# Kernel optimization log

Hardware: AMD Instinct MI355X
Metric: run time of the kernel (lower is better)

## Reference

```python
import jax, jax.numpy as jnp
import numpy as np

B, S, D, H = 2, 2048, 1024, 16
DK = D // H  # 64
ROPE_THETA = 10000.0


def apply_rope(t, positions):
    # t: [B, H, S, DK]; positions: [B, S]
    half = DK // 2
    inv_freq = 1.0 / (ROPE_THETA ** (jnp.arange(0, DK, 2, dtype=jnp.float32) / DK))  # [half]
    ang = positions.astype(jnp.float32)[:, None, :, None] * inv_freq  # [B,1,S,half]
    cos, sin = jnp.cos(ang), jnp.sin(ang)
    t_even = t[..., 0::2]
    t_odd = t[..., 1::2]
    r_even = t_even * cos - t_odd * sin
    r_odd = t_even * sin + t_odd * cos
    # interleave back to original layout
    return jnp.stack([r_even, r_odd], axis=-1).reshape(t.shape)


def setup_inputs() -> dict:
    key = jax.random.key(0)
    ks = jax.random.split(key, 5)
    x = jax.random.normal(ks[0], (B, S, D), dtype=jnp.float32)
    token_positions = jnp.broadcast_to(jnp.arange(S, dtype=jnp.int64 if jax.config.jax_enable_x64 else jnp.int32), (B, S))
    w_q = jax.random.normal(ks[1], (D, D), dtype=jnp.float32)
    w_k = jax.random.normal(ks[2], (D, D), dtype=jnp.float32)
    w_v = jax.random.normal(ks[3], (D, D), dtype=jnp.float32)
    w_o = jax.random.normal(ks[4], (D, D), dtype=jnp.float32)
    return {"x": x, "token_positions": token_positions, "w_q": w_q, "w_k": w_k, "w_v": w_v, "w_o": w_o}


def reference(x, token_positions, w_q, w_k, w_v, w_o):
    # project: weights stored as (h*d_k, d_model)
    wq = w_q.reshape(H, DK, D)
    wk = w_k.reshape(H, DK, D)
    wv = w_v.reshape(H, DK, D)
    q = jnp.einsum('bsd,hkd->bhsk', x, wq)  # [B,H,S,DK]
    k = jnp.einsum('bsd,hkd->bhsk', x, wk)
    v = jnp.einsum('bsd,hkd->bhsk', x, wv)
    q = apply_rope(q, token_positions)
    k = apply_rope(k, token_positions)
    scale = 1.0 / jnp.sqrt(jnp.float32(DK))
    scores = jnp.einsum('bhnk,bhmk->bhnm', q, k) * scale  # [B,H,S,S]
    causal = jnp.tril(jnp.ones((S, S), dtype=bool))
    scores = jnp.where(causal, scores, -jnp.inf)
    attn = jax.nn.softmax(scores, axis=-1)
    out = jnp.einsum('bhnm,bhmv->bhnv', attn, v)  # [B,H,S,DK]
    out = jnp.transpose(out, (0, 2, 1, 3)).reshape(B, S, H * DK)
    return jnp.einsum('bsf,df->bsd', out, w_o)
```

## Files before the change

### kernel.cpp

```cpp
#include <hip/hip_runtime.h>

typedef unsigned short u16;
typedef unsigned int u32;
typedef __attribute__((ext_vector_type(8))) __bf16 bf16x8;
typedef __attribute__((ext_vector_type(4))) float f32x4;

#define NSEQ 2048
#define NDIM 1024
#define NHEAD 16
#define NTOK 4096
#define NX   4194304
#define NWEL 1048576

__device__ __forceinline__ u16 f2bf(float f) {
  unsigned u = __float_as_uint(f);
  return (u16)((u + 0x7fffu + ((u >> 16) & 1u)) >> 16);
}
__device__ __forceinline__ float bf2f(u16 h) {
  return __uint_as_float(((unsigned)h) << 16);
}
__device__ __forceinline__ bf16x8 ld16(const u16* p) {
  int4 v = *reinterpret_cast<const int4*>(p);
  return __builtin_bit_cast(bf16x8, v);
}
__device__ __forceinline__ f32x4 mfma16(bf16x8 a, bf16x8 b, f32x4 c) {
  return __builtin_amdgcn_mfma_f32_16x16x32_bf16(a, b, c, 0, 0, 0);
}
__device__ __forceinline__ u32 cvtpk(float lo, float hi) {
  u32 r;
  asm("v_cvt_pk_bf16_f32 %0, %1, %2" : "=v"(r) : "v"(lo), "v"(hi));
  return r;
}
__device__ __forceinline__ void gload16(const u16* g, u16* l) {
  __builtin_amdgcn_global_load_lds(
      (const __attribute__((address_space(1))) void*)g,
      (__attribute__((address_space(3))) void*)l, 16, 0, 0);
}

#define GEMM_PROLOGUE                                                         \
  const int tid = threadIdx.x;                                                \
  const int lane = tid & 63, wid = tid >> 6;                                  \
  const int wm = wid >> 1, wn = wid & 1;                                      \
  const int lr = lane & 15, lg = lane >> 4;                                   \
  const int srow_ = tid >> 2;                                                 \
  const int sch_ = ((tid & 3) ^ ((tid >> 3) & 3)) * 8;                        \
  const int rsw_ = (lg ^ ((lr >> 1) & 3)) * 8;

#define STAGE3(BB, AH, AL, BH, BL, T0, J0, K0)                                \
  {                                                                           \
    u16* bb_ = (BB);                                                          \
    gload16(AH + (size_t)((T0) + srow_) * NDIM + (K0) + sch_, bb_ + tid * 8); \
    gload16(AH + (size_t)((T0) + 64 + srow_) * NDIM + (K0) + sch_,            \
            bb_ + 2048 + tid * 8);                                            \
    gload16(BH + (size_t)((J0) + srow_) * NDIM + (K0) + sch_,                 \
            bb_ + 4096 + tid * 8);                                            \
    gload16(BH + (size_t)((J0) + 64 + srow_) * NDIM + (K0) + sch_,            \
            bb_ + 6144 + tid * 8);                                            \
    gload16(AL + (size_t)((T0) + srow_) * NDIM + (K0) + sch_,                 \
            bb_ + 8192 + tid * 8);                                            \
    gload16(AL + (size_t)((T0) + 64 + srow_) * NDIM + (K0) + sch_,            \
            bb_ + 10240 + tid * 8);                                           \
    gload16(BL + (size_t)((J0) + srow_) * NDIM + (K0) + sch_,                 \
            bb_ + 12288 + tid * 8);                                           \
    gload16(BL + (size_t)((J0) + 64 + srow_) * NDIM + (K0) + sch_,            \
            bb_ + 14336 + tid * 8);                                           \
  }

#define GEMM3_LOOP(AH, AL, BH, BL, T0, J0)                                    \
  STAGE3(lds, AH, AL, BH, BL, T0, J0, 0)                                      \
  __syncthreads();                                                            \
  for (int k0 = 0; k0 < NDIM; k0 += 32) {                                     \
    u16* cb_ = lds + ((k0 >> 5) & 1) * 16384;                                 \
    if (k0 + 32 < NDIM) {                                                     \
      u16* nb_ = lds + ((((k0 >> 5) & 1) ^ 1) * 16384);                       \
      STAGE3(nb_, AH, AL, BH, BL, T0, J0, k0 + 32)                            \
    }                                                                         \
    bf16x8 afh[4], afl[4];                                                    \
    _Pragma("unroll") for (int m = 0; m < 4; m++) {                           \
      int off = (wm * 64 + m * 16 + lr) * 32 + rsw_;                          \
      afh[m] = ld16(cb_ + off);                                               \
      afl[m] = ld16(cb_ + 8192 + off);                                        \
    }                                                                         \
    _Pragma("unroll") for (int n = 0; n < 4; n++) {                           \
      int off = (wn * 64 + n * 16 + lr) * 32 + rsw_;                          \
      bf16x8 bfh = ld16(cb_ + 4096 + off);                                    \
      bf16x8 bfl = ld16(cb_ + 12288 + off);                                   \
      _Pragma("unroll") for (int m = 0; m < 4; m++) {                         \
        acc[m][n] = mfma16(afh[m], bfh, acc[m][n]);                           \
        acc[m][n] = mfma16(afh[m], bfl, acc[m][n]);                           \
        acc[m][n] = mfma16(afl[m], bfh, acc[m][n]);                           \
      }                                                                       \
    }                                                                         \
    __syncthreads();                                                          \
  }

#define STAGE1(BB, AH, BH, T0, J0, K0)                                        \
  {                                                                           \
    u16* bb_ = (BB);                                                          \
    gload16(AH + (size_t)((T0) + srow_) * NDIM + (K0) + sch_, bb_ + tid * 8); \
    gload16(AH + (size_t)((T0) + 64 + srow_) * NDIM + (K0) + sch_,            \
            bb_ + 2048 + tid * 8);                                            \
    gload16(BH + (size_t)((J0) + srow_) * NDIM + (K0) + sch_,                 \
            bb_ + 4096 + tid * 8);                                            \
    gload16(BH + (size_t)((J0) + 64 + srow_) * NDIM + (K0) + sch_,            \
            bb_ + 6144 + tid * 8);                                            \
  }

#define GEMM1_LOOP(AH, BH, T0, J0)                                            \
  STAGE1(lds, AH, BH, T0, J0, 0)                                              \
  __syncthreads();                                                            \
  for (int k0 = 0; k0 < NDIM; k0 += 32) {                                     \
    u16* cb_ = lds + ((k0 >> 5) & 1) * 8192;                                  \
    if (k0 + 32 < NDIM) {                                                     \
      u16* nb_ = lds + ((((k0 >> 5) & 1) ^ 1) * 8192);                        \
      STAGE1(nb_, AH, BH, T0, J0, k0 + 32)                                    \
    }                                                                         \
    bf16x8 afh[4];                                                            \
    _Pragma("unroll") for (int m = 0; m < 4; m++) {                           \
      int off = (wm * 64 + m * 16 + lr) * 32 + rsw_;                          \
      afh[m] = ld16(cb_ + off);                                               \
    }                                                                         \
    _Pragma("unroll") for (int n = 0; n < 4; n++) {                           \
      int off = (wn * 64 + n * 16 + lr) * 32 + rsw_;                          \
      bf16x8 bfh = ld16(cb_ + 4096 + off);                                    \
      _Pragma("unroll") for (int m = 0; m < 4; m++) {                         \
        acc[m][n] = mfma16(afh[m], bfh, acc[m][n]);                           \
      }                                                                       \
    }                                                                         \
    __syncthreads();                                                          \
  }

__global__ __launch_bounds__(256) void k_prep(
    const float* __restrict__ x, const float* __restrict__ wq,
    const float* __restrict__ wk, const float* __restrict__ wv,
    const float* __restrict__ wo,
    u16* __restrict__ xh, u16* __restrict__ xl,
    u16* __restrict__ wh, u16* __restrict__ wl) {
  int g = blockIdx.x * 256 + threadIdx.x;
  const float4* src;
  u16 *dh, *dl;
  int idx;
  bool wantlo = true;
  if (g < NX / 4) {
    src = (const float4*)x; dh = xh; dl = xl; idx = g;
  } else {
    int z = (g - NX / 4) / (NWEL / 4);
    int r = (g - NX / 4) % (NWEL / 4);
    src = (const float4*)(z == 0 ? wq : z == 1 ? wk : z == 2 ? wv : wo);
    dh = wh + (size_t)z * NWEL; dl = wl + (size_t)z * NWEL; idx = r;
    wantlo = (z < 2);
  }
  float4 v = src[idx];
  u16 h0 = f2bf(v.x), h1 = f2bf(v.y), h2 = f2bf(v.z), h3 = f2bf(v.w);
  ushort4 hv = make_ushort4(h0, h1, h2, h3);
  ((ushort4*)dh)[idx] = hv;
  if (wantlo) {
    ushort4 lv = make_ushort4(f2bf(v.x - bf2f(h0)), f2bf(v.y - bf2f(h1)),
                              f2bf(v.z - bf2f(h2)), f2bf(v.w - bf2f(h3)));
    ((ushort4*)dl)[idx] = lv;
  }
}

__global__ __launch_bounds__(256) void k_tab(float2* __restrict__ csn) {
  int idx = blockIdx.x * 256 + threadIdx.x;
  int p = idx >> 5, j = idx & 31;
  double invf = exp((double)(2 * j) * (-9.210340371976184 / 64.0));
  double ang = (double)p * invf;
  double kq = rint(ang * 0.15915494309189535);
  float a = (float)(ang - kq * 6.283185307179586);
  csn[idx] = make_float2(cosf(a), sinf(a));
}

__global__ __launch_bounds__(256) void k_qkv(
    const u16* __restrict__ xh, const u16* __restrict__ xl,
    const u16* __restrict__ wh, const u16* __restrict__ wl,
    const int* __restrict__ tokpos, const float2* __restrict__ csn,
    u16* __restrict__ qh, u16* __restrict__ ql,
    u16* __restrict__ kh, u16* __restrict__ kl) {
  __shared__ __align__(16) u16 lds[32768];
  const int z = blockIdx.z;
  const int t0 = blockIdx.y * 128, j0 = blockIdx.x * 128;
  const int h0 = j0 >> 6;
  GEMM_PROLOGUE
  const u16* Bh = wh + (size_t)z * NWEL;
  const u16* Bl = wl + (size_t)z * NWEL;
  f32x4 acc[4][4];
#pragma unroll
  for (int m = 0; m < 4; m++)
#pragma unroll
    for (int n = 0; n < 4; n++) acc[m][n] = f32x4{0.f, 0.f, 0.f, 0.f};
  GEMM3_LOOP(xh, xl, Bh, Bl, t0, j0)

  const int b = t0 >> 11, s0 = t0 & 2047;
  u16* dh = (z == 0) ? qh : kh;
  u16* dl = (z == 0) ? ql : kl;
  float rv[4][4][4];
#pragma unroll
  for (int m = 0; m < 4; m++) {
#pragma unroll
    for (int r = 0; r < 4; r++) {
      int pos = tokpos[t0 + wm * 64 + m * 16 + lg * 4 + r];
#pragma unroll
      for (int n = 0; n < 4; n++) {
        float val = acc[m][n][r];
        float nb = __shfl_xor(val, 1);
        int dk = (wn * 64 + n * 16 + lr) & 63;
        float2 cs = csn[pos * 32 + (dk >> 1)];
        rv[m][r][n] = (dk & 1) ? (nb * cs.y + val * cs.x)
                               : (val * cs.x - nb * cs.y);
      }
    }
  }
#pragma unroll
  for (int pass = 0; pass < 2; pass++) {
    __syncthreads();
#pragma unroll
    for (int m = 0; m < 4; m++)
#pragma unroll
      for (int r = 0; r < 4; r++) {
        int rloc = wm * 64 + m * 16 + lg * 4 + r;
#pragma unroll
        for (int n = 0; n < 4; n++) {
          int cloc = wn * 64 + n * 16 + lr;
          float v = rv[m][r][n];
          u16 hi = f2bf(v);
          lds[rloc * 128 + cloc] = pass == 0 ? hi : f2bf(v - bf2f(hi));
        }
      }
    __syncthreads();
    u16* dst = pass == 0 ? dh : dl;
#pragma unroll
    for (int i = 0; i < 8; i++) {
      int idx = tid + i * 256;
      int r = idx >> 4, cc = idx & 15;
      int4 v = *(int4*)(lds + r * 128 + cc * 8);
      int h2 = cc >> 3, dk = (cc & 7) * 8;
      size_t off = ((size_t)((b * NHEAD + h0 + h2) * NSEQ + s0 + r)) * 64 + dk;
      *(int4*)(dst + off) = v;
    }
  }
}

__global__ __launch_bounds__(256) void k_v(
    const u16* __restrict__ xh, const u16* __restrict__ wvh,
    u16* __restrict__ vt) {
  __shared__ __align__(16) u16 lds[16384];
  const int t0 = blockIdx.y * 128, j0 = blockIdx.x * 128;
  const int h0 = j0 >> 6;
  GEMM_PROLOGUE
  f32x4 acc[4][4];
#pragma unroll
  for (int m = 0; m < 4; m++)
#pragma unroll
    for (int n = 0; n < 4; n++) acc[m][n] = f32x4{0.f, 0.f, 0.f, 0.f};
  GEMM1_LOOP(xh, wvh, t0, j0)
  const int b = t0 >> 11, s0 = t0 & 2047;
#pragma unroll
  for (int m = 0; m < 4; m++)
#pragma unroll
    for (int r = 0; r < 4; r++) {
      int rloc = wm * 64 + m * 16 + lg * 4 + r;
#pragma unroll
      for (int n = 0; n < 4; n++) {
        int cloc = wn * 64 + n * 16 + lr;
        lds[cloc * 128 + (rloc ^ ((cloc & 15) << 3))] = f2bf(acc[m][n][r]);
      }
    }
  __syncthreads();
#pragma unroll
  for (int i = 0; i < 8; i++) {
    int idx = tid + i * 256;
    int col = idx >> 4, rc = idx & 15;
    int4 v = *(int4*)(lds + col * 128 + ((rc * 8) ^ ((col & 15) << 3)));
    int h2 = col >> 6, dk = col & 63;
    size_t off = ((size_t)((b * NHEAD + h0 + h2) * 64 + dk)) * NSEQ + s0 + rc * 8;
    *(int4*)(vt + off) = v;
  }
}

#define ATT_STAGE(SEL, KT)                                                    \
  _Pragma("unroll") for (int j_ = 0; j_ < 3; j_++) {                          \
    int seg_ = w * 3 + j_;                                                    \
    int ten_ = seg_ >> 3, sub_ = seg_ & 7;                                    \
    int row_ = sub_ * 8 + (lane >> 3);                                        \
    int sc_ = ((lane & 7) * 8) ^ ((row_ & 7) * 8);             \
    u16* dst_ = (ten_ == 0 ? &skh[SEL][0]                                     \
                           : ten_ == 1 ? &skl[SEL][0] : &svb[SEL][0]) +       \
                sub_ * 512;                                                   \
    const u16* src_ =                                                         \
        (ten_ == 2)                                                           \
            ? vt + vbase + (size_t)row_ * NSEQ + (KT) * 64 + sc_              \
            : (ten_ == 0 ? kh : kl) + base + (size_t)((KT) * 64 + row_) * 64 + sc_; \
    gload16(src_, dst_);                                                      \
  }

__global__ __launch_bounds__(512) void k_attn(
    const u16* __restrict__ qh, const u16* __restrict__ ql,
    const u16* __restrict__ kh, const u16* __restrict__ kl,
    const u16* __restrict__ vt, u16* __restrict__ ah) {
  __shared__ __align__(16) u16 skh[2][4096];
  __shared__ __align__(16) u16 skl[2][4096];
  __shared__ __align__(16) u16 svb[2][4096];
  __shared__ __align__(16) u16 sp[8192];
  const int tid = threadIdx.x, lane = tid & 63, w = tid >> 6;
  const int lr = lane & 15, lg = lane >> 4;
  const int wl4 = w & 3;
  const int fid = blockIdx.y * 16 + blockIdx.x;
  const int vb_ = (fid & 7) * 64 + (fid >> 3);
  const int bh = vb_ >> 4;
  const int qpair = vb_ & 15;
  const size_t base = (size_t)bh * NSEQ * 64;
  const size_t vbase = (size_t)bh * 64 * NSEQ;
  const int b = bh >> 4, h = bh & 15;
  const int qbA = 31 - qpair;
  const int myq = (w < 4) ? qbA : qpair;
  const int q0 = myq * 64;
  const int ntA = qbA + 1;
  const float SC2 = 0.18033688011112042f;

  const int qrow_g = q0 + wl4 * 16 + lr;
  bf16x8 qfh[2], qfl[2];
#pragma unroll
  for (int kk = 0; kk < 2; kk++) {
    qfh[kk] = ld16(qh + base + (size_t)qrow_g * 64 + kk * 32 + lg * 8);
    qfl[kk] = ld16(ql + base + (size_t)qrow_g * 64 + kk * 32 + lg * 8);
  }
  float mrun = -__builtin_inff(), lrun = 0.f;
  f32x4 oacc[4];
#pragma unroll
  for (int nf = 0; nf < 4; nf++) oacc[nf] = f32x4{0.f, 0.f, 0.f, 0.f};

  int sel = 0;
  ATT_STAGE(0, 0)
  __syncthreads();
  for (int kt = 0; kt < ntA; kt++) {
    if (kt + 1 < ntA) { ATT_STAGE(sel ^ 1, kt + 1) }
    if (kt <= myq) {
      f32x4 sacc[4];
#pragma unroll
      for (int nf = 0; nf < 4; nf++) sacc[nf] = f32x4{0.f, 0.f, 0.f, 0.f};
      __builtin_amdgcn_s_setprio(1);
#pragma unroll
      for (int nf = 0; nf < 4; nf++) {
        int krow = nf * 16 + lr;
        int swz = (krow & 7) * 8;
#pragma unroll
        for (int kk = 0; kk < 2; kk++) {
          int off = krow * 64 + ((kk * 32 + lg * 8) ^ swz);
          bf16x8 kfh = ld16(&skh[sel][0] + off);
          bf16x8 kfl = ld16(&skl[sel][0] + off);
          sacc[nf] = mfma16(kfh, qfh[kk], sacc[nf]);
          sacc[nf] = mfma16(kfl, qfh[kk], sacc[nf]);
          sacc[nf] = mfma16(kfh, qfl[kk], sacc[nf]);
        }
      }
      __builtin_amdgcn_s_setprio(0);
      float sv[4][4], mm[4];
#pragma unroll
      for (int nf = 0; nf < 4; nf++) {
#pragma unroll
        for (int r = 0; r < 4; r++) sv[nf][r] = sacc[nf][r] * SC2;
      }
      if (kt == myq) {
#pragma unroll
        for (int nf = 0; nf < 4; nf++)
#pragma unroll
          for (int r = 0; r < 4; r++) {
            int colg = kt * 64 + nf * 16 + lg * 4 + r;
            if (colg > qrow_g) sv[nf][r] = -__builtin_inff();
          }
      }
#pragma unroll
      for (int nf = 0; nf < 4; nf++)
        mm[nf] = fmaxf(fmaxf(sv[nf][0], sv[nf][1]), fmaxf(sv[nf][2], sv[nf][3]));
      float rmax = fmaxf(fmaxf(mm[0], mm[1]), fmaxf(mm[2], mm[3]));
      rmax = fmaxf(rmax, __shfl_xor(rmax, 16));
      rmax = fmaxf(rmax, __shfl_xor(rmax, 32));
      float alpha = 1.f;
      bool resc = __any(rmax > mrun + 8.f);
      if (resc) {
        float mnew = fmaxf(mrun, rmax);
        alpha = exp2f(mrun - mnew);
        mrun = mnew;
        lrun *= alpha;
      }
      float p[4][4];
      float ss[4];
#pragma unroll
      for (int nf = 0; nf < 4; nf++) {
#pragma unroll
        for (int r = 0; r < 4; r++) p[nf][r] = exp2f(sv[nf][r] - mrun);
        ss[nf] = (p[nf][0] + p[nf][1]) + (p[nf][2] + p[nf][3]);
      }
      float rsum = (ss[0] + ss[1]) + (ss[2] + ss[3]);
      rsum += __shfl_xor(rsum, 16);
      rsum += __shfl_xor(rsum, 32);
      lrun += rsum;
      {
        int prow = w * 16 + lr;
        int swz = (prow & 7) * 8;
#pragma unroll
        for (int nf = 0; nf < 4; nf++) {
          u32 w0 = cvtpk(p[nf][0], p[nf][1]);
          u32 w1 = cvtpk(p[nf][2], p[nf][3]);
          int col = (nf * 16 + lg * 4) ^ swz;
          *(uint2*)(&sp[prow * 64 + col]) = make_uint2(w0, w1);
        }
      }
      if (resc) {
        float af0 = __shfl(alpha, lg * 4 + 0);
        float af1 = __shfl(alpha, lg * 4 + 1);
        float af2 = __shfl(alpha, lg * 4 + 2);
        float af3 = __shfl(alpha, lg * 4 + 3);
#pragma unroll
        for (int nf = 0; nf < 4; nf++) {
          oacc[nf][0] *= af0; oacc[nf][1] *= af1;
          oacc[nf][2] *= af2; oacc[nf][3] *= af3;
        }
      }
      {
        int prow = w * 16 + lr;
        int pswz = (prow & 7) * 8;
        __builtin_amdgcn_s_setprio(1);
#pragma unroll
        for (int kk = 0; kk < 2; kk++) {
          bf16x8 pa = ld16(&sp[prow * 64 + ((kk * 32 + lg * 8) ^ pswz)]);
#pragma unroll
          for (int nf = 0; nf < 4; nf++) {
            int vrow = nf * 16 + lr;
            bf16x8 vb2 = ld16(&svb[sel][0] + vrow * 64 +
                              ((kk * 32 + lg * 8) ^ ((vrow & 7) * 8)));
            oacc[nf] = mfma16(pa, vb2, oacc[nf]);
          }
        }
        __builtin_amdgcn_s_setprio(0);
      }
    }
    __syncthreads();
    sel ^= 1;
  }
  float inv = 1.0f / lrun;
  float iv0 = __shfl(inv, lg * 4 + 0);
  float iv1 = __shfl(inv, lg * 4 + 1);
  float iv2 = __shfl(inv, lg * 4 + 2);
  float iv3 = __shfl(inv, lg * 4 + 3);
#pragma unroll
  for (int r = 0; r < 4; r++) {
    float ivr = r == 0 ? iv0 : r == 1 ? iv1 : r == 2 ? iv2 : iv3;
    int row = q0 + wl4 * 16 + lg * 4 + r;
    size_t toff = ((size_t)(b * NSEQ + row)) * NDIM + h * 64;
#pragma unroll
    for (int nf = 0; nf < 4; nf++) {
      ah[toff + nf * 16 + lr] = f2bf(oacc[nf][r] * ivr);
    }
  }
}

__global__ __launch_bounds__(256) void k_out(
    const u16* __restrict__ ah, const u16* __restrict__ wh,
    float* __restrict__ out) {
  __shared__ __align__(16) u16 lds[16384];
  const int t0 = blockIdx.y * 128, j0 = blockIdx.x * 128;
  GEMM_PROLOGUE
  f32x4 acc[4][4];
#pragma unroll
  for (int m = 0; m < 4; m++)
#pragma unroll
    for (int n = 0; n < 4; n++) acc[m][n] = f32x4{0.f, 0.f, 0.f, 0.f};
  GEMM1_LOOP(ah, wh, t0, j0)
#pragma unroll
  for (int m = 0; m < 4; m++)
#pragma unroll
    for (int r = 0; r < 4; r++) {
      int row = t0 + wm * 64 + m * 16 + lg * 4 + r;
#pragma unroll
      for (int n = 0; n < 4; n++) {
        int col = j0 + wn * 64 + n * 16 + lr;
        out[(size_t)row * NDIM + col] = acc[m][n][r];
      }
    }
}

extern "C" void kernel_launch(void* const* d_in, const int* in_sizes, int n_in,
                              void* d_out, int out_size, void* d_ws, size_t ws_size,
                              hipStream_t stream) {
  (void)in_sizes; (void)n_in; (void)out_size; (void)ws_size;
  const float* x = (const float*)d_in[0];
  const int* tokpos = (const int*)d_in[1];
  const float* wq = (const float*)d_in[2];
  const float* wk = (const float*)d_in[3];
  const float* wv = (const float*)d_in[4];
  const float* wo = (const float*)d_in[5];
  float* out = (float*)d_out;

  u16* ws = (u16*)d_ws;
  u16* xh = ws;
  u16* xl = xh + NX;
  u16* wh = xl + NX;
  u16* wl = wh + 4 * (size_t)NWEL;
  u16* qh = wl + 4 * (size_t)NWEL;
  u16* ql = qh + NX;
  u16* kh = ql + NX;
  u16* kl = kh + NX;
  u16* vt = kl + NX;
  float2* csn = (float2*)(vt + NX);

  k_prep<<<dim3(8192), dim3(256), 0, stream>>>(x, wq, wk, wv, wo, xh, xl, wh, wl);
  k_tab<<<dim3(256), dim3(256), 0, stream>>>(csn);
  k_qkv<<<dim3(8, 32, 2), dim3(256), 0, stream>>>(xh, xl, wh, wl, tokpos, csn,
                                                  qh, ql, kh, kl);
  k_v<<<dim3(8, 32), dim3(256), 0, stream>>>(xh, wh + 2 * (size_t)NWEL, vt);
  k_attn<<<dim3(16, 32), dim3(512), 0, stream>>>(qh, ql, kh, kl, vt, xh);
  k_out<<<dim3(8, 32), dim3(256), 0, stream>>>(xh, wh + 3 * (size_t)NWEL, out);
}
```

Measured before the change: 179.9 us.

## Fold softmax scale into Q, single-pass QK epilogue, incremental attention load pointers

The QK projection epilogue now scales Q by the softmax constant (including log2e) before the bf16 hi/lo split. It writes both hi and lo planes to LDS in one pass behind a single barrier, where before it kept an rv register array and made two passes with two barriers each. The attention kernel drops its per-score multiply, precomputes its staging source/dest pointers and advances them by a stride each tile, and uses v_max3 for row maxima. Pre-scaling Q before the bf16 split slightly changes rounding, and the epilogue's LDS footprint doubles to the full 32K-element buffer.

```diff
diff --git a/kernel.cpp b/kernel.cpp
--- a/kernel.cpp
+++ b/kernel.cpp
@@ -30,6 +30,11 @@
   u32 r;
   asm("v_cvt_pk_bf16_f32 %0, %1, %2" : "=v"(r) : "v"(lo), "v"(hi));
   return r;
+}
+__device__ __forceinline__ float max3f(float a, float b, float c) {
+  float d;
+  asm("v_max3_f32 %0, %1, %2, %3" : "=v"(d) : "v"(a), "v"(b), "v"(c));
+  return d;
 }
 __device__ __forceinline__ void gload16(const u16* g, u16* l) {
   __builtin_amdgcn_global_load_lds(
@@ -194,50 +199,39 @@
   const int b = t0 >> 11, s0 = t0 & 2047;
   u16* dh = (z == 0) ? qh : kh;
   u16* dl = (z == 0) ? ql : kl;
-  float rv[4][4][4];
+  const float scl = (z == 0) ? 0.18033688011112042f : 1.0f;
 #pragma unroll
   for (int m = 0; m < 4; m++) {
 #pragma unroll
     for (int r = 0; r < 4; r++) {
       int pos = tokpos[t0 + wm * 64 + m * 16 + lg * 4 + r];
+      int rloc = wm * 64 + m * 16 + lg * 4 + r;
 #pragma unroll
       for (int n = 0; n < 4; n++) {
         float val = acc[m][n][r];
         float nb = __shfl_xor(val, 1);
         int dk = (wn * 64 + n * 16 + lr) & 63;
         float2 cs = csn[pos * 32 + (dk >> 1)];
-        rv[m][r][n] = (dk & 1) ? (nb * cs.y + val * cs.x)
-                               : (val * cs.x - nb * cs.y);
+        float v = ((dk & 1) ? (nb * cs.y + val * cs.x)
+                            : (val * cs.x - nb * cs.y)) * scl;
+        int cloc = wn * 64 + n * 16 + lr;
+        u16 hi = f2bf(v);
+        lds[rloc * 128 + cloc] = hi;
+        lds[16384 + rloc * 128 + cloc] = f2bf(v - bf2f(hi));
       }
     }
   }
-#pragma unroll
-  for (int pass = 0; pass < 2; pass++) {
-    __syncthreads();
-#pragma unroll
-    for (int m = 0; m < 4; m++)
-#pragma unroll
-      for (int r = 0; r < 4; r++) {
-        int rloc = wm * 64 + m * 16 + lg * 4 + r;
-#pragma unroll
-        for (int n = 0; n < 4; n++) {
-          int cloc = wn * 64 + n * 16 + lr;
-          float v = rv[m][r][n];
-          u16 hi = f2bf(v);
-          lds[rloc * 128 + cloc] = pass == 0 ? hi : f2bf(v - bf2f(hi));
-        }
-      }
-    __syncthreads();
-    u16* dst = pass == 0 ? dh : dl;
-#pragma unroll
-    for (int i = 0; i < 8; i++) {
-      int idx = tid + i * 256;
-      int r = idx >> 4, cc = idx & 15;
-      int4 v = *(int4*)(lds + r * 128 + cc * 8);
-      int h2 = cc >> 3, dk = (cc & 7) * 8;
-      size_t off = ((size_t)((b * NHEAD + h0 + h2) * NSEQ + s0 + r)) * 64 + dk;
-      *(int4*)(dst + off) = v;
-    }
+  __syncthreads();
+#pragma unroll
+  for (int i = 0; i < 16; i++) {
+    int idx = tid + i * 256;
+    int plane = idx >> 11, i2 = idx & 2047;
+    int r = i2 >> 4, cc = i2 & 15;
+    int4 v = *(int4*)(lds + plane * 16384 + r * 128 + cc * 8);
+    int h2 = cc >> 3, dk = (cc & 7) * 8;
+    u16* dst = plane ? dl : dh;
+    size_t off = ((size_t)((b * NHEAD + h0 + h2) * NSEQ + s0 + r)) * 64 + dk;
+    *(int4*)(dst + off) = v;
   }
 }
 
@@ -278,20 +272,10 @@
   }
 }
 
-#define ATT_STAGE(SEL, KT)                                                    \
+#define ATT_STAGE(SEL)                                                        \
   _Pragma("unroll") for (int j_ = 0; j_ < 3; j_++) {                          \
-    int seg_ = w * 3 + j_;                                                    \
-    int ten_ = seg_ >> 3, sub_ = seg_ & 7;                                    \
-    int row_ = sub_ * 8 + (lane >> 3);                                        \
-    int sc_ = ((lane & 7) * 8) ^ ((row_ & 7) * 8);             \
-    u16* dst_ = (ten_ == 0 ? &skh[SEL][0]                                     \
-                           : ten_ == 1 ? &skl[SEL][0] : &svb[SEL][0]) +       \
-                sub_ * 512;                                                   \
-    const u16* src_ =                                                         \
-        (ten_ == 2)                                                           \
-            ? vt + vbase + (size_t)row_ * NSEQ + (KT) * 64 + sc_              \
-            : (ten_ == 0 ? kh : kl) + base + (size_t)((KT) * 64 + row_) * 64 + sc_; \
-    gload16(src_, dst_);                                                      \
+    gload16(asrc[j_], adst[j_] + (SEL) * 4096);                               \
+    asrc[j_] += astr[j_];                                                     \
   }
 
 __global__ __launch_bounds__(512) void k_attn(
@@ -316,7 +300,6 @@
   const int myq = (w < 4) ? qbA : qpair;
   const int q0 = myq * 64;
   const int ntA = qbA + 1;
-  const float SC2 = 0.18033688011112042f;
 
   const int qrow_g = q0 + wl4 * 16 + lr;
   bf16x8 qfh[2], qfl[2];
@@ -330,11 +313,28 @@
 #pragma unroll
   for (int nf = 0; nf < 4; nf++) oacc[nf] = f32x4{0.f, 0.f, 0.f, 0.f};
 
+  const u16* asrc[3];
+  u16* adst[3];
+  int astr[3];
+#pragma unroll
+  for (int j_ = 0; j_ < 3; j_++) {
+    int seg_ = w * 3 + j_;
+    int ten_ = seg_ >> 3, sub_ = seg_ & 7;
+    int row_ = sub_ * 8 + (lane >> 3);
+    int sc_ = ((lane & 7) * 8) ^ ((row_ & 7) * 8);
+    adst[j_] = (ten_ == 0 ? &skh[0][0] : ten_ == 1 ? &skl[0][0] : &svb[0][0]) +
+               sub_ * 512;
+    astr[j_] = (ten_ == 2) ? 64 : 4096;
+    asrc[j_] = (ten_ == 2)
+                   ? vt + vbase + (size_t)row_ * NSEQ + sc_
+                   : (ten_ == 0 ? kh : kl) + base + (size_t)row_ * 64 + sc_;
+  }
+
   int sel = 0;
-  ATT_STAGE(0, 0)
+  ATT_STAGE(0)
   __syncthreads();
   for (int kt = 0; kt < ntA; kt++) {
-    if (kt + 1 < ntA) { ATT_STAGE(sel ^ 1, kt + 1) }
+    if (kt + 1 < ntA) { ATT_STAGE(sel ^ 1) }
     if (kt <= myq) {
       f32x4 sacc[4];
 #pragma unroll
@@ -359,7 +359,7 @@
 #pragma unroll
       for (int nf = 0; nf < 4; nf++) {
 #pragma unroll
-        for (int r = 0; r < 4; r++) sv[nf][r] = sacc[nf][r] * SC2;
+        for (int r = 0; r < 4; r++) sv[nf][r] = sacc[nf][r];
       }
       if (kt == myq) {
 #pragma unroll
@@ -372,8 +372,8 @@
       }
 #pragma unroll
       for (int nf = 0; nf < 4; nf++)
-        mm[nf] = fmaxf(fmaxf(sv[nf][0], sv[nf][1]), fmaxf(sv[nf][2], sv[nf][3]));
-      float rmax = fmaxf(fmaxf(mm[0], mm[1]), fmaxf(mm[2], mm[3]));
+        mm[nf] = fmaxf(max3f(sv[nf][0], sv[nf][1], sv[nf][2]), sv[nf][3]);
+      float rmax = fmaxf(max3f(mm[0], mm[1], mm[2]), mm[3]);
       rmax = fmaxf(rmax, __shfl_xor(rmax, 16));
       rmax = fmaxf(rmax, __shfl_xor(rmax, 32));
       float alpha = 1.f;
```

Result: faster. 173.5 us (-3.6%).
